# Optimization experiments

Measured on AMD Instinct MI355X. Metric: run time of the kernel, lower is better.

The kernel has to match this reference:

```python
import jax, jax.numpy as jnp
import numpy as np

DICE_TH = 0.4
CLS_TH = 0.5
LN_EPS = 1e-5


def setup_inputs() -> dict:
    key = jax.random.key(0)
    P, C, NC, K = 200_000, 256, 200, 24  # points, clicks, classes, latent prototypes
    ks = jax.random.split(key, 6)
    # structured masks: each click targets one of K prototype regions so the
    # dice/cls thresholds yield a non-degenerate grouping
    point_proto = jax.random.randint(ks[0], (P,), 0, K)
    proto_vals = jax.random.uniform(ks[1], (P,))
    click_proto = jax.random.randint(ks[2], (C,), 0, K)
    base = (point_proto[:, None] == click_proto[None, :]).astype(jnp.float32)  # [P, C]
    noise = jax.random.uniform(ks[3], (P, C))
    masks_heatmap = base * (0.6 + 0.4 * proto_vals[:, None]) + 0.02 * noise
    class_emb = jax.random.normal(ks[4], (K, NC)) * 3.0
    cls_logits = class_emb[click_proto] + 0.3 * jax.random.normal(ks[5], (C, NC))
    clicks_list = jax.random.randint(ks[0], (C,), 0, NC)  # unused (random_clicks=True)
    return {"masks_heatmap": masks_heatmap, "cls_logits": cls_logits,
            "clicks_list": clicks_list}


def _associate(masks_heatmap, cls_logits):
    """Greedy dice+cls-similarity grouping (random_clicks=True path).
    Returns labels[c] = leader click index of the group containing click c."""
    M = masks_heatmap                      # [P, C]
    C = M.shape[1]
    s = M.sum(0)                           # [C]
    # dice[i, j] = 2 * m_i . m_j / (sum(m_i) + sum(m_j))  (all pairs at once)
    dice = 2.0 * (M.T @ M) / (s[:, None] + s[None, :])
    # F.layer_norm over last dim, no affine
    mu = cls_logits.mean(-1, keepdims=True)
    var = ((cls_logits - mu) ** 2).mean(-1, keepdims=True)
    p = (cls_logits - mu) / jnp.sqrt(var + LN_EPS)
    sim = p @ p.T                          # [C, C]
    cond = (dice > DICE_TH) & (sim > CLS_TH)

    def step(carry, x):
        assigned, labels = carry
        i, row = x
        # skip if i already suppressed; take unsuppressed clicks matching row i
        take = row & (~assigned) & (~assigned[i])
        return (assigned | take, jnp.where(take, i, labels)), None

    init = (jnp.zeros((C,), bool), jnp.full((C,), -1, jnp.int32))
    (assigned, labels), _ = jax.lax.scan(
        step, init, (jnp.arange(C, dtype=jnp.int32), cond))
    return labels


def _merge(labels, masks_heatmap, cls_logits):
    """reduction='max': per-group max over member clicks. Unused group slots
    (non-leader indices) are zero-filled and flagged by group_valid."""
    C = masks_heatmap.shape[1]
    seg = jnp.where(labels >= 0, labels, C)  # route unassigned to dump segment
    counts = jax.ops.segment_sum(jnp.ones((C,), jnp.float32), seg,
                                 num_segments=C + 1)[:C]
    group_valid = counts > 0
    nm = jax.ops.segment_max(masks_heatmap.T, seg, num_segments=C + 1)[:C]  # [C, P]
    nc = jax.ops.segment_max(cls_logits, seg, num_segments=C + 1)[:C]      # [C, NC]
    new_masks = jnp.where(group_valid[:, None], nm, 0.0).T  # [P, C]
    new_cls = jnp.where(group_valid[:, None], nc, 0.0)      # [C, NC]
    return new_masks, new_cls, group_valid


def reference(masks_heatmap, cls_logits, clicks_list):
    labels = _associate(masks_heatmap, cls_logits)
    new_masks, new_cls, group_valid = _merge(labels, masks_heatmap, cls_logits)
    return labels, group_valid, new_masks, new_cls
```

## Files before the change

kernel.cpp:

```cpp
#include <hip/hip_runtime.h>
#include <cstdint>
#include <cstddef>

constexpr int P  = 200000;
constexpr int C  = 256;
constexpr int NC = 200;
#define DICE_TH 0.4f
#define CLS_TH  0.5f
#define LN_EPS  1e-5f

constexpr int KC = 1600;
constexpr int NCHUNK = 125;

constexpr size_t WS_G       = 0;
constexpr size_t WS_S       = 262144;
constexpr size_t WS_PROW    = 263168;
constexpr size_t WS_PT      = 467968;
constexpr size_t WS_COND    = 672768;
constexpr size_t WS_MSTART  = 680960;
constexpr size_t WS_MEMBERS = 682240;

typedef float floatx16 __attribute__((ext_vector_type(16)));
typedef __bf16 bf16x8 __attribute__((ext_vector_type(8)));
typedef unsigned short ushort8 __attribute__((ext_vector_type(8)));

__device__ __forceinline__ unsigned short f2bf(float f) {
  unsigned u = __builtin_bit_cast(unsigned, f);
  unsigned r = u + 0x7FFFu + ((u >> 16) & 1u);
  return (unsigned short)(r >> 16);
}

constexpr int LDA = 40;

__global__ __launch_bounds__(256, 2) void gram_mfma_kernel(
    const float* __restrict__ M, float* __restrict__ G, float* __restrict__ s) {
  __shared__ unsigned short Abf[128 * LDA];
  __shared__ unsigned short Bbf[128 * LDA];

  const int type = blockIdx.x;
  const int i0 = (type == 2) ? 128 : 0;
  const int j0 = (type == 0) ? 0 : 128;
  const bool diag = (type != 1);
  const int tid = threadIdx.x;
  const int wv = tid >> 6, lane = tid & 63;
  const int c = tid & 127, h = tid >> 7;
  const int k0 = blockIdx.y * KC;

  floatx16 acc[4];
#pragma unroll
  for (int t = 0; t < 4; ++t)
#pragma unroll
    for (int r = 0; r < 16; ++r) acc[t][r] = 0.f;
  float ssum = 0.f;

  const int mrow = lane & 31;
  const int kgrp = (lane >> 5) * 8;

  for (int step = 0; step < KC / 32; ++step) {
    const int kb = k0 + step * 32 + h * 16;
    {
      const float* col = M + (size_t)kb * 256 + i0 + c;
      float v[16];
#pragma unroll
      for (int u = 0; u < 16; ++u) v[u] = col[(size_t)u * 256];
      if (diag) {
#pragma unroll
        for (int u = 0; u < 16; ++u) ssum += v[u];
      }
      ushort8 lo, hi;
#pragma unroll
      for (int u = 0; u < 8; ++u) { lo[u] = f2bf(v[u]); hi[u] = f2bf(v[u + 8]); }
      *reinterpret_cast<ushort8*>(&Abf[c * LDA + h * 16]) = lo;
      *reinterpret_cast<ushort8*>(&Abf[c * LDA + h * 16 + 8]) = hi;
    }
    if (!diag) {
      const float* col = M + (size_t)kb * 256 + j0 + c;
      float v[16];
#pragma unroll
      for (int u = 0; u < 16; ++u) v[u] = col[(size_t)u * 256];
      ushort8 lo, hi;
#pragma unroll
      for (int u = 0; u < 8; ++u) { lo[u] = f2bf(v[u]); hi[u] = f2bf(v[u + 8]); }
      *reinterpret_cast<ushort8*>(&Bbf[c * LDA + h * 16]) = lo;
      *reinterpret_cast<ushort8*>(&Bbf[c * LDA + h * 16 + 8]) = hi;
    }
    __syncthreads();

    const unsigned short* Bsrc = diag ? Abf : Bbf;
#pragma unroll
    for (int sub = 0; sub < 2; ++sub) {
      const int ko = sub * 16 + kgrp;
      bf16x8 a = __builtin_bit_cast(
          bf16x8, *reinterpret_cast<const ushort8*>(
                      &Abf[(32 * wv + mrow) * LDA + ko]));
#pragma unroll
      for (int t = 0; t < 4; ++t) {
        bf16x8 b = __builtin_bit_cast(
            bf16x8, *reinterpret_cast<const ushort8*>(
                        &Bsrc[(32 * t + mrow) * LDA + ko]));
        acc[t] = __builtin_amdgcn_mfma_f32_32x32x16_bf16(a, b, acc[t], 0, 0, 0);
      }
    }
    __syncthreads();
  }

#pragma unroll
  for (int t = 0; t < 4; ++t) {
    const int gc = j0 + 32 * t + (lane & 31);
#pragma unroll
    for (int r = 0; r < 16; ++r) {
      const int gr = i0 + 32 * wv + (r & 3) + 8 * (r >> 2) + 4 * (lane >> 5);
      atomicAdd(&G[(size_t)gr * 256 + gc], acc[t][r]);
    }
  }
  if (diag) atomicAdd(&s[i0 + c], ssum);
}

__global__ __launch_bounds__(64) void ln_kernel(const float* __restrict__ cls,
                                                float* __restrict__ p_row,
                                                float* __restrict__ pT) {
  const int c = blockIdx.x;
  const int t = threadIdx.x;
  const float* x = cls + (size_t)c * NC;
  float v0 = x[t];
  float v1 = x[t + 64];
  float v2 = (t < 72) ? x[t + 128] : 0.f;

  float sum = v0 + v1 + v2;
#pragma unroll
  for (int o = 32; o > 0; o >>= 1) sum += __shfl_xor(sum, o);
  const float mu = sum / (float)NC;

  float d0 = v0 - mu, d1 = v1 - mu, d2 = (t < 72) ? (v2 - mu) : 0.f;
  float sq = d0 * d0 + d1 * d1 + d2 * d2;
#pragma unroll
  for (int o = 32; o > 0; o >>= 1) sq += __shfl_xor(sq, o);
  const float var = sq / (float)NC;
  const float inv = 1.0f / sqrtf(var + LN_EPS);

  float p0 = d0 * inv, p1 = d1 * inv, p2 = d2 * inv;
  p_row[(size_t)c * NC + t] = p0;
  p_row[(size_t)c * NC + t + 64] = p1;
  pT[(size_t)t * C + c] = p0;
  pT[(size_t)(t + 64) * C + c] = p1;
  if (t < 72) {
    p_row[(size_t)c * NC + t + 128] = p2;
    pT[(size_t)(t + 128) * C + c] = p2;
  }
}

__global__ __launch_bounds__(256) void cond_kernel(
    const float* __restrict__ G, const float* __restrict__ s,
    const float* __restrict__ p_row, const float* __restrict__ pT,
    unsigned long long* __restrict__ condW) {
  __shared__ float pi[NC];
  const int i = blockIdx.x;
  const int j = threadIdx.x;
  if (j < NC) pi[j] = p_row[(size_t)i * NC + j];
  __syncthreads();

  const float si = s[i];
  const float sj = s[j];
  const float g = (i >= 128 && j < 128) ? G[(size_t)j * C + i]
                                        : G[(size_t)i * C + j];
  const float dice = 2.f * g / (si + sj);

  float acc = 0.f;
#pragma unroll 8
  for (int k = 0; k < NC; ++k) acc = fmaf(pi[k], pT[(size_t)k * C + j], acc);

  const bool cnd = (dice > DICE_TH) && (acc > CLS_TH);
  unsigned long long m = __ballot(cnd);
  if ((j & 63) == 0) condW[i * 4 + (j >> 6)] = m;
}

__global__ __launch_bounds__(64) void scan_kernel(
    const unsigned long long* __restrict__ condW,
    float* __restrict__ out_labels, float* __restrict__ out_valid,
    int* __restrict__ mstart, int* __restrict__ members) {
  __shared__ unsigned long long cS[C * 4];
  __shared__ int cnt[C];
  __shared__ int ms[C + 1];
  const int t = threadIdx.x;

  for (int idx = t; idx < C * 4; idx += 64) cS[idx] = condW[idx];
  for (int idx = t; idx < C; idx += 64) cnt[idx] = 0;
  __syncthreads();

  unsigned long long asg[4] = {0ull, 0ull, 0ull, 0ull};
  int lab[4] = {-1, -1, -1, -1};

#pragma unroll
  for (int w = 0; w < 4; ++w) {
    for (int b = 0; b < 64; ++b) {
      const int i = w * 64 + b;
      if (!((asg[w] >> b) & 1ull)) {
#pragma unroll
        for (int w2 = 0; w2 < 4; ++w2) {
          unsigned long long tk = cS[i * 4 + w2] & ~asg[w2];
          asg[w2] |= tk;
          if ((tk >> t) & 1ull) lab[w2] = i;
        }
      }
    }
  }

#pragma unroll
  for (int w = 0; w < 4; ++w)
    if (lab[w] >= 0) atomicAdd(&cnt[lab[w]], 1);
  __syncthreads();

  if (t == 0) {
    ms[0] = 0;
    for (int c2 = 0; c2 < C; ++c2) ms[c2 + 1] = ms[c2] + cnt[c2];
  }
  __syncthreads();
  for (int idx = t; idx < C; idx += 64) cnt[idx] = ms[idx];
  __syncthreads();
#pragma unroll
  for (int w = 0; w < 4; ++w) {
    if (lab[w] >= 0) {
      int pos = atomicAdd(&cnt[lab[w]], 1);
      members[pos] = w * 64 + t;
    }
  }
#pragma unroll
  for (int w = 0; w < 4; ++w) {
    const int col = w * 64 + t;
    out_labels[col] = (float)lab[w];
    out_valid[col] = (ms[col + 1] > ms[col]) ? 1.0f : 0.0f;
  }
  for (int idx = t; idx < C + 1; idx += 64) mstart[idx] = ms[idx];
}

__global__ __launch_bounds__(256) void merge_masks_kernel(
    const float* __restrict__ M, const int* __restrict__ mstart,
    const int* __restrict__ members, float* __restrict__ out_masks) {
  __shared__ float rows[8 * 256];
  __shared__ int msS[C + 1];
  __shared__ int memS[C];
  const int tid = threadIdx.x;
  const size_t p0 = (size_t)blockIdx.x * 8;

  msS[tid] = mstart[tid];
  if (tid == 0) msS[C] = mstart[C];
  memS[tid] = members[tid];

  const float4* src = reinterpret_cast<const float4*>(M + p0 * 256);
#pragma unroll
  for (int it = 0; it < 2; ++it)
    reinterpret_cast<float4*>(rows)[it * 256 + tid] = src[it * 256 + tid];
  __syncthreads();

  const int st = msS[tid], en = msS[tid + 1];
  float mx[8];
  if (en > st) {
    const int m0 = memS[st];
#pragma unroll
    for (int r = 0; r < 8; ++r) mx[r] = rows[r * 256 + m0];
    for (int k = st + 1; k < en; ++k) {
      const int mm = memS[k];
#pragma unroll
      for (int r = 0; r < 8; ++r) mx[r] = fmaxf(mx[r], rows[r * 256 + mm]);
    }
  } else {
#pragma unroll
    for (int r = 0; r < 8; ++r) mx[r] = 0.f;
  }
#pragma unroll
  for (int r = 0; r < 8; ++r) out_masks[(p0 + r) * 256 + tid] = mx[r];
}

__global__ __launch_bounds__(256) void merge_cls_kernel(
    const float* __restrict__ cls, const int* __restrict__ mstart,
    const int* __restrict__ members, float* __restrict__ out_cls) {
  __shared__ int se[2];
  const int c = blockIdx.x;
  const int t = threadIdx.x;
  if (t < 2) se[t] = mstart[c + t];
  __syncthreads();
  const int st = se[0], en = se[1];
  if (t < NC) {
    float mx = 0.f;
    if (en > st) {
      mx = cls[(size_t)members[st] * NC + t];
      for (int k = st + 1; k < en; ++k)
        mx = fmaxf(mx, cls[(size_t)members[k] * NC + t]);
    }
    out_cls[(size_t)c * NC + t] = mx;
  }
}

extern "C" void kernel_launch(void* const* d_in, const int* in_sizes, int n_in,
                              void* d_out, int out_size, void* d_ws,
                              size_t ws_size, hipStream_t stream) {
  const float* M = (const float*)d_in[0];
  const float* cls = (const float*)d_in[1];

  float* out = (float*)d_out;
  char* ws = (char*)d_ws;
  float* G = (float*)(ws + WS_G);
  float* s = (float*)(ws + WS_S);
  float* p_row = (float*)(ws + WS_PROW);
  float* pT = (float*)(ws + WS_PT);
  unsigned long long* condW = (unsigned long long*)(ws + WS_COND);
  int* mstart = (int*)(ws + WS_MSTART);
  int* members = (int*)(ws + WS_MEMBERS);

  float* out_labels = out;
  float* out_valid = out + 256;
  float* out_masks = out + 512;
  float* out_cls = out + 512 + (size_t)P * 256;

  hipMemsetAsync(ws, 0, WS_S + 1024, stream);

  gram_mfma_kernel<<<dim3(3, NCHUNK), 256, 0, stream>>>(M, G, s);
  ln_kernel<<<C, 64, 0, stream>>>(cls, p_row, pT);
  cond_kernel<<<C, 256, 0, stream>>>(G, s, p_row, pT, condW);
  scan_kernel<<<1, 64, 0, stream>>>(condW, out_labels, out_valid, mstart,
                                    members);
  merge_masks_kernel<<<P / 8, 256, 0, stream>>>(M, mstart, members, out_masks);
  merge_cls_kernel<<<C, 256, 0, stream>>>(cls, mstart, members, out_cls);
}
```

Measured before the change: 454.6 us.

## Prefetch gram tiles into registers, split K finer, unroll scan and merges

The gram kernel now loads the next 32-row slab of M into registers while the MFMAs for the current slab run, so global latency overlaps compute. The K chunk is halved to double the grid, which adds more atomic or partial accumulation into G and s. Separately, the cond kernel's dot product uses four independent accumulators, the scan kernel's greedy loop is flattened with next-row prefetch from shared memory, and the merge-masks kernel handles 16 rows per block instead of 8. The extra prefetch registers and larger per-thread arrays raise register pressure.

```diff
diff --git a/kernel.cpp b/kernel.cpp
--- a/kernel.cpp
+++ b/kernel.cpp
@@ -9,8 +9,9 @@
 #define CLS_TH  0.5f
 #define LN_EPS  1e-5f
 
-constexpr int KC = 1600;
-constexpr int NCHUNK = 125;
+constexpr int KC = 800;
+constexpr int NCHUNK = 250;
+constexpr int NSTEP = KC / 32;
 
 constexpr size_t WS_G       = 0;
 constexpr size_t WS_S       = 262144;
@@ -56,35 +57,49 @@
   const int mrow = lane & 31;
   const int kgrp = (lane >> 5) * 8;
 
-  for (int step = 0; step < KC / 32; ++step) {
-    const int kb = k0 + step * 32 + h * 16;
+  float va[16], vb[16];
+  {
+    const float* colA = M + (size_t)(k0 + h * 16) * 256 + i0 + c;
+#pragma unroll
+    for (int u = 0; u < 16; ++u) va[u] = colA[(size_t)u * 256];
+    if (!diag) {
+      const float* colB = M + (size_t)(k0 + h * 16) * 256 + j0 + c;
+#pragma unroll
+      for (int u = 0; u < 16; ++u) vb[u] = colB[(size_t)u * 256];
+    }
+  }
+
+  for (int step = 0; step < NSTEP; ++step) {
     {
-      const float* col = M + (size_t)kb * 256 + i0 + c;
-      float v[16];
-#pragma unroll
-      for (int u = 0; u < 16; ++u) v[u] = col[(size_t)u * 256];
       if (diag) {
 #pragma unroll
-        for (int u = 0; u < 16; ++u) ssum += v[u];
+        for (int u = 0; u < 16; ++u) ssum += va[u];
       }
       ushort8 lo, hi;
 #pragma unroll
-      for (int u = 0; u < 8; ++u) { lo[u] = f2bf(v[u]); hi[u] = f2bf(v[u + 8]); }
+      for (int u = 0; u < 8; ++u) { lo[u] = f2bf(va[u]); hi[u] = f2bf(va[u + 8]); }
       *reinterpret_cast<ushort8*>(&Abf[c * LDA + h * 16]) = lo;
       *reinterpret_cast<ushort8*>(&Abf[c * LDA + h * 16 + 8]) = hi;
-    }
-    if (!diag) {
-      const float* col = M + (size_t)kb * 256 + j0 + c;
-      float v[16];
-#pragma unroll
-      for (int u = 0; u < 16; ++u) v[u] = col[(size_t)u * 256];
-      ushort8 lo, hi;
-#pragma unroll
-      for (int u = 0; u < 8; ++u) { lo[u] = f2bf(v[u]); hi[u] = f2bf(v[u + 8]); }
-      *reinterpret_cast<ushort8*>(&Bbf[c * LDA + h * 16]) = lo;
-      *reinterpret_cast<ushort8*>(&Bbf[c * LDA + h * 16 + 8]) = hi;
+      if (!diag) {
+#pragma unroll
+        for (int u = 0; u < 8; ++u) { lo[u] = f2bf(vb[u]); hi[u] = f2bf(vb[u + 8]); }
+        *reinterpret_cast<ushort8*>(&Bbf[c * LDA + h * 16]) = lo;
+        *reinterpret_cast<ushort8*>(&Bbf[c * LDA + h * 16 + 8]) = hi;
+      }
     }
     __syncthreads();
+
+    if (step + 1 < NSTEP) {
+      const int kb = k0 + (step + 1) * 32 + h * 16;
+      const float* colA = M + (size_t)kb * 256 + i0 + c;
+#pragma unroll
+      for (int u = 0; u < 16; ++u) va[u] = colA[(size_t)u * 256];
+      if (!diag) {
+        const float* colB = M + (size_t)kb * 256 + j0 + c;
+#pragma unroll
+        for (int u = 0; u < 16; ++u) vb[u] = colB[(size_t)u * 256];
+      }
+    }
 
     const unsigned short* Bsrc = diag ? Abf : Bbf;
 #pragma unroll
@@ -165,9 +180,15 @@
                                         : G[(size_t)i * C + j];
   const float dice = 2.f * g / (si + sj);
 
-  float acc = 0.f;
-#pragma unroll 8
-  for (int k = 0; k < NC; ++k) acc = fmaf(pi[k], pT[(size_t)k * C + j], acc);
+  float a0 = 0.f, a1 = 0.f, a2 = 0.f, a3 = 0.f;
+#pragma unroll 2
+  for (int k = 0; k < NC; k += 4) {
+    a0 = fmaf(pi[k + 0], pT[(size_t)(k + 0) * C + j], a0);
+    a1 = fmaf(pi[k + 1], pT[(size_t)(k + 1) * C + j], a1);
+    a2 = fmaf(pi[k + 2], pT[(size_t)(k + 2) * C + j], a2);
+    a3 = fmaf(pi[k + 3], pT[(size_t)(k + 3) * C + j], a3);
+  }
+  const float acc = (a0 + a1) + (a2 + a3);
 
   const bool cnd = (dice > DICE_TH) && (acc > CLS_TH);
   unsigned long long m = __ballot(cnd);
@@ -190,19 +211,20 @@
   unsigned long long asg[4] = {0ull, 0ull, 0ull, 0ull};
   int lab[4] = {-1, -1, -1, -1};
 
-#pragma unroll
-  for (int w = 0; w < 4; ++w) {
-    for (int b = 0; b < 64; ++b) {
-      const int i = w * 64 + b;
-      if (!((asg[w] >> b) & 1ull)) {
-#pragma unroll
-        for (int w2 = 0; w2 < 4; ++w2) {
-          unsigned long long tk = cS[i * 4 + w2] & ~asg[w2];
-          asg[w2] |= tk;
-          if ((tk >> t) & 1ull) lab[w2] = i;
-        }
-      }
-    }
+  unsigned long long r0 = cS[0], r1 = cS[1], r2 = cS[2], r3 = cS[3];
+  for (int i = 0; i < C; ++i) {
+    const int nx = (i + 1 < C) ? (i + 1) * 4 : 0;
+    unsigned long long n0 = cS[nx], n1 = cS[nx + 1], n2 = cS[nx + 2],
+                       n3 = cS[nx + 3];
+    const int w = i >> 6, b = i & 63;
+    if (!((asg[w] >> b) & 1ull)) {
+      unsigned long long tk;
+      tk = r0 & ~asg[0]; asg[0] |= tk; if ((tk >> t) & 1ull) lab[0] = i;
+      tk = r1 & ~asg[1]; asg[1] |= tk; if ((tk >> t) & 1ull) lab[1] = i;
+      tk = r2 & ~asg[2]; asg[2] |= tk; if ((tk >> t) & 1ull) lab[2] = i;
+      tk = r3 & ~asg[3]; asg[3] |= tk; if ((tk >> t) & 1ull) lab[3] = i;
+    }
+    r0 = n0; r1 = n1; r2 = n2; r3 = n3;
   }
 
 #pragma unroll
@@ -236,11 +258,11 @@
 __global__ __launch_bounds__(256) void merge_masks_kernel(
     const float* __restrict__ M, const int* __restrict__ mstart,
     const int* __restrict__ members, float* __restrict__ out_masks) {
-  __shared__ float rows[8 * 256];
+  __shared__ float rows[16 * 256];
   __shared__ int msS[C + 1];
   __shared__ int memS[C];
   const int tid = threadIdx.x;
-  const size_t p0 = (size_t)blockIdx.x * 8;
+  const size_t p0 = (size_t)blockIdx.x * 16;
 
   msS[tid] = mstart[tid];
   if (tid == 0) msS[C] = mstart[C];
@@ -248,27 +270,27 @@
 
   const float4* src = reinterpret_cast<const float4*>(M + p0 * 256);
 #pragma unroll
-  for (int it = 0; it < 2; ++it)
+  for (int it = 0; it < 4; ++it)
     reinterpret_cast<float4*>(rows)[it * 256 + tid] = src[it * 256 + tid];
   __syncthreads();
 
   const int st = msS[tid], en = msS[tid + 1];
-  float mx[8];
+  float mx[16];
   if (en > st) {
     const int m0 = memS[st];
 #pragma unroll
-    for (int r = 0; r < 8; ++r) mx[r] = rows[r * 256 + m0];
+    for (int r = 0; r < 16; ++r) mx[r] = rows[r * 256 + m0];
     for (int k = st + 1; k < en; ++k) {
       const int mm = memS[k];
 #pragma unroll
-      for (int r = 0; r < 8; ++r) mx[r] = fmaxf(mx[r], rows[r * 256 + mm]);
+      for (int r = 0; r < 16; ++r) mx[r] = fmaxf(mx[r], rows[r * 256 + mm]);
     }
   } else {
 #pragma unroll
-    for (int r = 0; r < 8; ++r) mx[r] = 0.f;
-  }
-#pragma unroll
-  for (int r = 0; r < 8; ++r) out_masks[(p0 + r) * 256 + tid] = mx[r];
+    for (int r = 0; r < 16; ++r) mx[r] = 0.f;
+  }
+#pragma unroll
+  for (int r = 0; r < 16; ++r) out_masks[(p0 + r) * 256 + tid] = mx[r];
 }
 
 __global__ __launch_bounds__(256) void merge_cls_kernel(
@@ -319,6 +341,6 @@
   cond_kernel<<<C, 256, 0, stream>>>(G, s, p_row, pT, condW);
   scan_kernel<<<1, 64, 0, stream>>>(condW, out_labels, out_valid, mstart,
                                     members);
-  merge_masks_kernel<<<P / 8, 256, 0, stream>>>(M, mstart, members, out_masks);
+  merge_masks_kernel<<<P / 16, 256, 0, stream>>>(M, mstart, members, out_masks);
   merge_cls_kernel<<<C, 256, 0, stream>>>(cls, mstart, members, out_cls);
 }
```

Result: slower. 464.1 us (+2.1%).
